# Optimization experiments

Measured on AMD Instinct MI355X. Metric: run time of the kernel, lower is better.

Reference implementation:

```python
import jax, jax.numpy as jnp
import numpy as np

TAU = 1.0
LOSS_WEIGHT = 1.0
N = 4_000_000


def setup_inputs() -> dict:
    key = jax.random.key(0)
    k1, k2 = jax.random.split(key)

    def make_boxes(k):
        u = jax.random.uniform(k, (N, 5), dtype=jnp.float32)
        xy = u[:, :2] * 1024.0                 # centers in a 1024px image
        wh = u[:, 2:4] * 100.0 + 4.0           # box sizes in [4, 104)
        r = (u[:, 4:5] - 0.5) * jnp.pi         # angle in [-pi/2, pi/2)
        return jnp.concatenate([xy, wh, r], axis=-1)

    return {"pred": make_boxes(k1), "target": make_boxes(k2)}


def xy_wh_r_2_xy_sigma(xywhr):
    """(N,5) rbox -> (mu (N,2), sigma (N,2,2)) via R @ (S/2)^2 @ R^T closed form."""
    xy = xywhr[..., :2]
    wh = jnp.clip(xywhr[..., 2:4], 1e-7, 1e7)
    r = xywhr[..., 4]
    c, s = jnp.cos(r), jnp.sin(r)
    a = (0.5 * wh[..., 0]) ** 2  # (w/2)^2
    b = (0.5 * wh[..., 1]) ** 2  # (h/2)^2
    s00 = a * c * c + b * s * s
    s11 = a * s * s + b * c * c
    s01 = (a - b) * s * c
    sigma = jnp.stack(
        [jnp.stack([s00, s01], -1), jnp.stack([s01, s11], -1)], -2
    )  # (N,2,2)
    return xy, sigma


def _det2(m):
    return m[..., 0, 0] * m[..., 1, 1] - m[..., 0, 1] * m[..., 1, 0]


def _inv2(m):
    det = _det2(m)
    adj = jnp.stack(
        [jnp.stack([m[..., 1, 1], -m[..., 0, 1]], -1),
         jnp.stack([-m[..., 1, 0], m[..., 0, 0]], -1)], -2)
    return adj / det[..., None, None]


def kld_loss(mu_p, sigma_p, mu_t, sigma_t, tau):
    delta = mu_p - mu_t                                # (N,2)
    sigma_t_inv = _inv2(sigma_t)                       # (N,2,2)
    # delta^T Sigma_t^{-1} delta
    term1 = jnp.einsum('ni,nij,nj->n', delta, sigma_t_inv, delta)
    # tr(Sigma_t^{-1} Sigma_p) + log(det Sigma_t / det Sigma_p)
    tr = jnp.einsum('nij,nji->n', sigma_t_inv, sigma_p)
    term2 = tr + jnp.log(_det2(sigma_t) / _det2(sigma_p))
    dis = term1 + term2 - 2.0
    kl_dis = jnp.maximum(dis, 1e-6)
    # fun == 'log1p'
    loss = 1.0 - 1.0 / (tau + jnp.log1p(kl_dis))
    return loss[:, None]                               # (N,1) like torch version


def reference(pred, target):
    mu_p, sigma_p = xy_wh_r_2_xy_sigma(pred)
    mu_t, sigma_t = xy_wh_r_2_xy_sigma(target)
    return kld_loss(mu_p, sigma_p, mu_t, sigma_t, TAU) * LOSS_WEIGHT
```

## Files before the change

kernel.cpp:

```cpp
#include <hip/hip_runtime.h>
#include <math.h>

#ifndef TAU_CONST
#define TAU_CONST 1.0f
#endif

__device__ __forceinline__ void rbox_to_gauss(float x, float y, float w, float h, float r,
                                              float& mx, float& my,
                                              float& s00, float& s01, float& s11, float& det) {
    w = fminf(fmaxf(w, 1e-7f), 1e7f);
    h = fminf(fmaxf(h, 1e-7f), 1e7f);
    float a = 0.25f * w * w;
    float b = 0.25f * h * h;
    float s, c;
    __sincosf(r, &s, &c);
    s00 = a * c * c + b * s * s;
    s11 = a * s * s + b * c * c;
    s01 = (a - b) * s * c;
    det = s00 * s11 - s01 * s01;
    mx = x; my = y;
}

__device__ __forceinline__ float kld_row(const float* p, const float* t) {
    float pmx, pmy, p00, p01, p11, dp;
    float tmx, tmy, t00, t01, t11, dt;
    rbox_to_gauss(p[0], p[1], p[2], p[3], p[4], pmx, pmy, p00, p01, p11, dp);
    rbox_to_gauss(t[0], t[1], t[2], t[3], t[4], tmx, tmy, t00, t01, t11, dt);
    float dx = pmx - tmx, dy = pmy - tmy;
    float inv_dt = 1.0f / dt;
    float term1 = (dx * dx * t11 - 2.0f * dx * dy * t01 + dy * dy * t00) * inv_dt;
    float tr = (t11 * p00 + t00 * p11 - 2.0f * t01 * p01) * inv_dt;
    float term2 = tr + logf(dt / dp);
    float dis = term1 + term2 - 2.0f;
    float kl = fmaxf(dis, 1e-6f);
    return 1.0f - 1.0f / (TAU_CONST + log1pf(kl));
}

__global__ void __launch_bounds__(256) gdloss_vec4_kernel(const float* __restrict__ pred,
                                                          const float* __restrict__ target,
                                                          float* __restrict__ out, int n4) {
    int tid = blockIdx.x * blockDim.x + threadIdx.x;
    if (tid >= n4) return;
    const float4* pp = (const float4*)pred;
    const float4* tp = (const float4*)target;
    float4 pv[5], tv[5];
#pragma unroll
    for (int k = 0; k < 5; ++k) {
        pv[k] = pp[5 * tid + k];
        tv[k] = tp[5 * tid + k];
    }
    const float* pf = (const float*)pv;
    const float* tf = (const float*)tv;
    float4 o;
    o.x = kld_row(pf + 0,  tf + 0);
    o.y = kld_row(pf + 5,  tf + 5);
    o.z = kld_row(pf + 10, tf + 10);
    o.w = kld_row(pf + 15, tf + 15);
    ((float4*)out)[tid] = o;
}

__global__ void gdloss_tail_kernel(const float* __restrict__ pred,
                                   const float* __restrict__ target,
                                   float* __restrict__ out, int start, int n) {
    int i = start + blockIdx.x * blockDim.x + threadIdx.x;
    if (i >= n) return;
    float p[5], t[5];
#pragma unroll
    for (int k = 0; k < 5; ++k) {
        p[k] = pred[5 * i + k];
        t[k] = target[5 * i + k];
    }
    out[i] = kld_row(p, t);
}

extern "C" void kernel_launch(void* const* d_in, const int* in_sizes, int n_in,
                              void* d_out, int out_size, void* d_ws, size_t ws_size,
                              hipStream_t stream) {
    const float* pred   = (const float*)d_in[0];
    const float* target = (const float*)d_in[1];
    float* out = (float*)d_out;
    int n = in_sizes[0] / 5;
    int n4 = n / 4;
    if (n4 > 0) {
        int blocks = (n4 + 255) / 256;
        gdloss_vec4_kernel<<<blocks, 256, 0, stream>>>(pred, target, out, n4);
    }
    int rem = n - n4 * 4;
    if (rem > 0) {
        gdloss_tail_kernel<<<1, 64, 0, stream>>>(pred, target, out, n4 * 4, n);
    }
}
```

Baseline: 178.4 us.

## Stage inputs through LDS for coalesced loads and use fast log/rcp intrinsics

Each block now loads its pred/target rows as contiguous float4 chunks strided by thread into shared memory. Each thread then reads its 20 floats back from LDS, replacing the old per-thread strided 5-float4 global loads with fully coalesced accesses. The math also switches to hardware reciprocal and __logf, and computes log1p as log(1+x), which trades some accuracy for fewer instructions. Staging adds LDS traffic, a barrier and possible bank conflicts on the 20-float strided LDS reads.

New measurement: 179.6 us. About the same (+0.7%).

```diff
diff --git a/kernel.cpp b/kernel.cpp
--- a/kernel.cpp
+++ b/kernel.cpp
@@ -1,62 +1,71 @@
 #include <hip/hip_runtime.h>
 #include <math.h>
 
-#ifndef TAU_CONST
 #define TAU_CONST 1.0f
-#endif
+#define BLOCK 256
+#define RPT 4
+#define RPB (BLOCK * RPT)
+#define F4PB (RPB * 5 / 4)
 
-__device__ __forceinline__ void rbox_to_gauss(float x, float y, float w, float h, float r,
-                                              float& mx, float& my,
-                                              float& s00, float& s01, float& s11, float& det) {
-    w = fminf(fmaxf(w, 1e-7f), 1e7f);
-    h = fminf(fmaxf(h, 1e-7f), 1e7f);
-    float a = 0.25f * w * w;
-    float b = 0.25f * h * h;
-    float s, c;
-    __sincosf(r, &s, &c);
-    s00 = a * c * c + b * s * s;
-    s11 = a * s * s + b * c * c;
-    s01 = (a - b) * s * c;
-    det = s00 * s11 - s01 * s01;
-    mx = x; my = y;
+__device__ __forceinline__ float fast_rcp(float x) { return __builtin_amdgcn_rcpf(x); }
+
+__device__ __forceinline__ float kld_row(const float* p, const float* t) {
+    float pw = fminf(fmaxf(p[2], 1e-7f), 1e7f), ph = fminf(fmaxf(p[3], 1e-7f), 1e7f);
+    float tw = fminf(fmaxf(t[2], 1e-7f), 1e7f), th = fminf(fmaxf(t[3], 1e-7f), 1e7f);
+    float ap = 0.25f * pw * pw, bp = 0.25f * ph * ph;
+    float at = 0.25f * tw * tw, bt = 0.25f * th * th;
+    float sp_, cp_; __sincosf(p[4], &sp_, &cp_);
+    float st_, ct_; __sincosf(t[4], &st_, &ct_);
+    float p00 = ap * cp_ * cp_ + bp * sp_ * sp_;
+    float p11 = ap * sp_ * sp_ + bp * cp_ * cp_;
+    float p01 = (ap - bp) * sp_ * cp_;
+    float t00 = at * ct_ * ct_ + bt * st_ * st_;
+    float t11 = at * st_ * st_ + bt * ct_ * ct_;
+    float t01 = (at - bt) * st_ * ct_;
+    float dp = p00 * p11 - p01 * p01;
+    float dt = t00 * t11 - t01 * t01;
+    float dx = p[0] - t[0], dy = p[1] - t[1];
+    float inv_dt = fast_rcp(dt);
+    float term1 = (dx * dx * t11 - 2.0f * dx * dy * t01 + dy * dy * t00) * inv_dt;
+    float tr    = (t11 * p00 + t00 * p11 - 2.0f * t01 * p01) * inv_dt;
+    float term2 = tr + (__logf(dt) - __logf(dp));
+    float dis = term1 + term2 - 2.0f;
+    float kl = fmaxf(dis, 1e-6f);
+    return 1.0f - fast_rcp(TAU_CONST + __logf(1.0f + kl));
 }
 
-__device__ __forceinline__ float kld_row(const float* p, const float* t) {
-    float pmx, pmy, p00, p01, p11, dp;
-    float tmx, tmy, t00, t01, t11, dt;
-    rbox_to_gauss(p[0], p[1], p[2], p[3], p[4], pmx, pmy, p00, p01, p11, dp);
-    rbox_to_gauss(t[0], t[1], t[2], t[3], t[4], tmx, tmy, t00, t01, t11, dt);
-    float dx = pmx - tmx, dy = pmy - tmy;
-    float inv_dt = 1.0f / dt;
-    float term1 = (dx * dx * t11 - 2.0f * dx * dy * t01 + dy * dy * t00) * inv_dt;
-    float tr = (t11 * p00 + t00 * p11 - 2.0f * t01 * p01) * inv_dt;
-    float term2 = tr + logf(dt / dp);
-    float dis = term1 + term2 - 2.0f;
-    float kl = fmaxf(dis, 1e-6f);
-    return 1.0f - 1.0f / (TAU_CONST + log1pf(kl));
-}
-
-__global__ void __launch_bounds__(256) gdloss_vec4_kernel(const float* __restrict__ pred,
-                                                          const float* __restrict__ target,
-                                                          float* __restrict__ out, int n4) {
-    int tid = blockIdx.x * blockDim.x + threadIdx.x;
-    if (tid >= n4) return;
-    const float4* pp = (const float4*)pred;
-    const float4* tp = (const float4*)target;
-    float4 pv[5], tv[5];
+__global__ void __launch_bounds__(BLOCK) gdloss_lds_kernel(const float4* __restrict__ pred4,
+                                                           const float4* __restrict__ targ4,
+                                                           float4* __restrict__ out4,
+                                                           int nf4_in, int n4_out) {
+    __shared__ float4 sP[F4PB];
+    __shared__ float4 sT[F4PB];
+    const int tid = threadIdx.x;
+    const int base4 = blockIdx.x * F4PB;
 #pragma unroll
     for (int k = 0; k < 5; ++k) {
-        pv[k] = pp[5 * tid + k];
-        tv[k] = tp[5 * tid + k];
+        int g = base4 + k * BLOCK + tid;
+        float4 v, u;
+        if (g < nf4_in) { v = pred4[g]; u = targ4[g]; }
+        else            { v = float4{0, 0, 0, 0}; u = float4{0, 0, 0, 0}; }
+        sP[k * BLOCK + tid] = v;
+        sT[k * BLOCK + tid] = u;
     }
-    const float* pf = (const float*)pv;
-    const float* tf = (const float*)tv;
+    __syncthreads();
+    const float4* pRow = (const float4*)((const float*)sP + 20 * tid);
+    const float4* tRow = (const float4*)((const float*)sT + 20 * tid);
+    float4 lp[5], lt[5];
+#pragma unroll
+    for (int k = 0; k < 5; ++k) { lp[k] = pRow[k]; lt[k] = tRow[k]; }
+    const float* P = (const float*)lp;
+    const float* T = (const float*)lt;
     float4 o;
-    o.x = kld_row(pf + 0,  tf + 0);
-    o.y = kld_row(pf + 5,  tf + 5);
-    o.z = kld_row(pf + 10, tf + 10);
-    o.w = kld_row(pf + 15, tf + 15);
-    ((float4*)out)[tid] = o;
+    o.x = kld_row(P + 0,  T + 0);
+    o.y = kld_row(P + 5,  T + 5);
+    o.z = kld_row(P + 10, T + 10);
+    o.w = kld_row(P + 15, T + 15);
+    int o4 = blockIdx.x * BLOCK + tid;
+    if (o4 < n4_out) out4[o4] = o;
 }
 
 __global__ void gdloss_tail_kernel(const float* __restrict__ pred,
@@ -66,10 +75,7 @@
     if (i >= n) return;
     float p[5], t[5];
 #pragma unroll
-    for (int k = 0; k < 5; ++k) {
-        p[k] = pred[5 * i + k];
-        t[k] = target[5 * i + k];
-    }
+    for (int k = 0; k < 5; ++k) { p[k] = pred[5 * i + k]; t[k] = target[5 * i + k]; }
     out[i] = kld_row(p, t);
 }
 
@@ -79,14 +85,16 @@
     const float* pred   = (const float*)d_in[0];
     const float* target = (const float*)d_in[1];
     float* out = (float*)d_out;
-    int n = in_sizes[0] / 5;
-    int n4 = n / 4;
+    const int n = in_sizes[0] / 5;
+    const int n4 = n / 4;
+    const int nf4_in = (n * 5) / 4;
     if (n4 > 0) {
-        int blocks = (n4 + 255) / 256;
-        gdloss_vec4_kernel<<<blocks, 256, 0, stream>>>(pred, target, out, n4);
+        int blocks = (n4 + BLOCK - 1) / BLOCK;
+        gdloss_lds_kernel<<<blocks, BLOCK, 0, stream>>>((const float4*)pred,
+                                                        (const float4*)target,
+                                                        (float4*)out, nf4_in, n4);
     }
-    int rem = n - n4 * 4;
-    if (rem > 0) {
+    if (n - n4 * 4 > 0) {
         gdloss_tail_kernel<<<1, 64, 0, stream>>>(pred, target, out, n4 * 4, n);
     }
 }
```
